# Optimization experiments

Measured on AMD Instinct MI355X. Metric: run time of the kernel, lower is better.

Reference implementation:

```python
import jax, jax.numpy as jnp
import numpy as np

E = 64          # num_experts
TOPK = 8        # num_experts_per_tok
I = 512         # moe_intermediate_size
H = 1024        # hidden_size
G = 128         # awq group_size
T = 2048        # tokens (batch*seq)

# AWQ nibble unpack order: bit shifts [0,16,4,20,8,24,12,28] -> indices [0,4,1,5,2,6,3,7]
_AWQ_SHIFTS = jnp.array([0, 4, 1, 5, 2, 6, 3, 7], dtype=jnp.int32) * 4


def awq_dequant(qw, qz, scales, group_size=G):
    """qw: (K, N//8) int32, qz: (K//G, N//8) int32, scales: (K//G, N) float.
    Returns dense weight (K, N): (q - z) * scale with per-group zero/scale."""
    K = qw.shape[0]
    uq = ((qw[:, :, None] >> _AWQ_SHIFTS) & 0xF).reshape(K, -1)          # (K, N)
    uz = ((qz[:, :, None] >> _AWQ_SHIFTS) & 0xF).reshape(qz.shape[0], -1)  # (K//G, N)
    uz = jnp.repeat(uz, group_size, axis=0)                               # (K, N)
    sc = jnp.repeat(scales, group_size, axis=0)                           # (K, N)
    return (uq.astype(scales.dtype) - uz.astype(scales.dtype)) * sc


def setup_inputs() -> dict:
    key = jax.random.key(0)
    ks = jax.random.split(key, 8)
    imax = 2**31 - 1
    return {
        "x": jax.random.normal(ks[0], (T, H), dtype=jnp.float32),
        "gate_w": jax.random.normal(ks[1], (E, H), dtype=jnp.float32) * 0.02,
        "qweight1": jax.random.randint(ks[2], (H, (E * I) // 8), 0, imax, dtype=jnp.int32),
        "qzeros1": jax.random.randint(ks[3], (H // G, (E * I) // 8), 0, imax, dtype=jnp.int32),
        "scales1": jax.random.normal(ks[4], (H // G, E * I), dtype=jnp.float32) * 0.02,
        "qweight2": jax.random.randint(ks[5], (I, (E * H) // 8), 0, imax, dtype=jnp.int32),
        "qzeros2": jax.random.randint(ks[6], (I // G, (E * H) // 8), 0, imax, dtype=jnp.int32),
        "scales2": jax.random.normal(ks[7], (I // G, E * H), dtype=jnp.float32) * 0.02,
    }


def reference(x, gate_w, qweight1, qzeros1, scales1, qweight2, qzeros2, scales2):
    # dequant grouped expert weights
    w1 = awq_dequant(qweight1, qzeros1, scales1).T.reshape(E, I, H)   # (E, I, H)
    w2 = awq_dequant(qweight2, qzeros2, scales2).T.reshape(E, H, I)   # (E, H, I)

    # routing: softmax -> top-k -> renormalize
    logits = x @ gate_w.T                                             # (T, E)
    probs = jax.nn.softmax(logits, axis=-1)
    topv, topi = jax.lax.top_k(probs, TOPK)                           # (T, K)
    topv = topv / jnp.sum(topv, axis=-1, keepdims=True)
    cw = jnp.sum(jax.nn.one_hot(topi, E, dtype=x.dtype) * topv[..., None], axis=1)  # (T, E)

    # experts: out = sum_e cw[t,e] * silu(x @ w1[e].T) @ w2[e].T
    h = jax.nn.silu(jnp.einsum('th,eih->tei', x, w1))                 # (T, E, I)
    h = h * cw[:, :, None]                                            # fold combine weights
    out = jnp.einsum('tei,ehi->th', h, w2)                            # (T, H)
    return out
```

## Files before the change

kernel.cpp:

```cpp
#include <hip/hip_runtime.h>
#include <hip/hip_bf16.h>

#define T_TOK 2048
#define HID   1024
#define EXP   64
#define TOPK  8
#define IMED  512
#define N1 (EXP * IMED)
#define C1 (N1 / 8)
#define N2 (EXP * HID)
#define C2 (N2 / 8)
#define MAXTILES 320

typedef _Float16 h16x2 __attribute__((ext_vector_type(2)));
typedef _Float16 h16x8 __attribute__((ext_vector_type(8)));
typedef float f32x4 __attribute__((ext_vector_type(4)));
typedef unsigned short ushortx4 __attribute__((ext_vector_type(4)));
typedef unsigned short ushortx8 __attribute__((ext_vector_type(8)));

__constant__ int kShifts[8] = {0, 16, 4, 20, 8, 24, 12, 28};

__device__ __forceinline__ void async16(const void* g, void* l) {
  __builtin_amdgcn_global_load_lds((const __attribute__((address_space(1))) void*)g,
                                   (__attribute__((address_space(3))) void*)l, 16, 0, 0);
}

__device__ __forceinline__ unsigned short f2h(float f) {
  return __builtin_bit_cast(unsigned short, (_Float16)f);
}
__device__ __forceinline__ float h2f(unsigned short b) {
  return (float)__builtin_bit_cast(_Float16, b);
}

__device__ __forceinline__ h16x8 unpack8h(unsigned q, h16x2 sh2, h16x2 zh2) {
  union { unsigned u[4]; h16x8 v; } out;
#pragma unroll
  for (int j = 0; j < 4; ++j) {
    const unsigned m = ((q >> (4 * j)) & 0x000F000Fu) | 0x64006400u;
    h16x2 d = __builtin_bit_cast(h16x2, m) - zh2;
    d = d * sh2;
    out.u[j] = __builtin_bit_cast(unsigned, d);
  }
  return out.v;
}

__device__ __forceinline__ void repack_body(const int* __restrict__ qw,
                                            unsigned* __restrict__ qk, int K, int C,
                                            int gx, int pp, int tid) {
  const int t = pp >> 2, fq = pp & 3;
  const int c2 = gx * 512 + tid * 2;
  const int nblk = c2 >> 1;
  unsigned o0[16], o1[16];
#pragma unroll
  for (int i = 0; i < 16; ++i) { o0[i] = 0u; o1[i] = 0u; }
  const int k0a = t * 64 + fq * 8;
  const int k0b = t * 64 + (fq + 4) * 8;
#pragma unroll
  for (int r = 0; r < 8; ++r) {
    const int2 va = *reinterpret_cast<const int2*>(qw + (size_t)(k0a + r) * C + c2);
    const int2 vb = *reinterpret_cast<const int2*>(qw + (size_t)(k0b + r) * C + c2);
    const int outsh = (r & 1) * 16 + (r >> 1) * 4;
    const unsigned qa[2] = {(unsigned)va.x, (unsigned)va.y};
    const unsigned qb[2] = {(unsigned)vb.x, (unsigned)vb.y};
#pragma unroll
    for (int ci = 0; ci < 2; ++ci) {
#pragma unroll
      for (int j = 0; j < 8; ++j) {
        const int sh = kShifts[j];
        o0[ci * 8 + j] |= ((qa[ci] >> sh) & 0xFu) << outsh;
        o1[ci * 8 + j] |= ((qb[ci] >> sh) & 0xFu) << outsh;
      }
    }
  }
  unsigned* dst = qk + (size_t)nblk * 2 * K + t * 128 + fq * 32;
#pragma unroll
  for (int idx = 0; idx < 16; ++idx)
    *reinterpret_cast<uint2*>(dst + idx * 2) = make_uint2(o0[idx], o1[idx]);
}

__global__ __launch_bounds__(256) void prep_kernel(
    const float* __restrict__ x, const float* __restrict__ gate_w,
    unsigned short* __restrict__ xh, float* __restrict__ partial,
    const int* __restrict__ qw1, unsigned* __restrict__ qk1,
    const int* __restrict__ qw2, unsigned* __restrict__ qk2,
    int* __restrict__ counts) {
  const int bid = blockIdx.x;
  const int tid = threadIdx.x;
  if (bid == 1535 && tid < 64) counts[tid] = 0;
  if (bid < 512) {
    __shared__ float xs[64][64];
    __shared__ float gs[64][64];
    const int t0 = (bid & 31) * 64;
    const int ks = bid >> 5;
    const int k0 = ks * 64;
    const int lrow = tid >> 4;
    const int cblk = tid & 15;
#pragma unroll
    for (int r = 0; r < 4; ++r) {
      const int row = r * 16 + lrow;
      const int sc = (cblk ^ ((row >> 2) & 15)) * 4;
      float4 xv = *reinterpret_cast<const float4*>(x + (size_t)(t0 + row) * HID + k0 + cblk * 4);
      float4 gv = *reinterpret_cast<const float4*>(gate_w + (size_t)row * HID + k0 + cblk * 4);
      *reinterpret_cast<float4*>(&xs[row][sc]) = xv;
      *reinterpret_cast<float4*>(&gs[row][sc]) = gv;
      ushortx4 o;
      o[0] = f2h(xv.x); o[1] = f2h(xv.y); o[2] = f2h(xv.z); o[3] = f2h(xv.w);
      *reinterpret_cast<ushortx4*>(xh + (size_t)(t0 + row) * HID + k0 + cblk * 4) = o;
    }
    __syncthreads();
    const int tg = (tid >> 4) * 4, eg = (tid & 15) * 4;
    const int xsw = tid >> 4, gsw = tid & 15;
    float acc[4][4] = {{0.f, 0.f, 0.f, 0.f}};
#pragma unroll 4
    for (int c = 0; c < 16; ++c) {
      float4 a[4], b[4];
#pragma unroll
      for (int i = 0; i < 4; ++i)
        a[i] = *reinterpret_cast<const float4*>(&xs[tg + i][(c ^ xsw) * 4]);
#pragma unroll
      for (int j = 0; j < 4; ++j)
        b[j] = *reinterpret_cast<const float4*>(&gs[eg + j][(c ^ gsw) * 4]);
#pragma unroll
      for (int i = 0; i < 4; ++i)
#pragma unroll
        for (int j = 0; j < 4; ++j) {
          acc[i][j] = fmaf(a[i].x, b[j].x, acc[i][j]);
          acc[i][j] = fmaf(a[i].y, b[j].y, acc[i][j]);
          acc[i][j] = fmaf(a[i].z, b[j].z, acc[i][j]);
          acc[i][j] = fmaf(a[i].w, b[j].w, acc[i][j]);
        }
    }
    float* dst = partial + ((size_t)ks * T_TOK + t0) * EXP;
#pragma unroll
    for (int i = 0; i < 4; ++i)
      *reinterpret_cast<float4*>(dst + (tg + i) * EXP + eg) =
          make_float4(acc[i][0], acc[i][1], acc[i][2], acc[i][3]);
  } else if (bid < 1024) {
    const int id = bid - 512;
    repack_body(qw1, qk1, HID, C1, id & 7, id >> 3, tid);
  } else {
    const int id = bid - 1024;
    repack_body(qw2, qk2, IMED, C2, id & 15, id >> 4, tid);
  }
}

__global__ __launch_bounds__(256) void topk_kernel(
    const float* __restrict__ partial, int* __restrict__ counts,
    int* __restrict__ tok_list, int* __restrict__ hslot_list,
    float* __restrict__ cw_list) {
  const int wave = threadIdx.x >> 6, lane = threadIdx.x & 63;
  const int t = blockIdx.x * 4 + wave;
  float lg = 0.f;
#pragma unroll
  for (int s = 0; s < 16; ++s)
    lg += partial[((size_t)s * T_TOK + t) * EXP + lane];

  float m = lg;
  for (int off = 32; off; off >>= 1) m = fmaxf(m, __shfl_xor(m, off));
  float pe = expf(lg - m);
  float s = pe;
  for (int off = 32; off; off >>= 1) s += __shfl_xor(s, off);
  float prob = pe / s;

  float pcur = prob;
  float myv = 0.f;
  int myi = -1;
  float tsum = 0.f;
  for (int k = 0; k < TOPK; ++k) {
    float vv = pcur;
    int idx = lane;
    for (int off = 32; off; off >>= 1) {
      float ov = __shfl_xor(vv, off);
      int oi = __shfl_xor(idx, off);
      if (ov > vv || (ov == vv && oi < idx)) { vv = ov; idx = oi; }
    }
    tsum += vv;
    if (lane == k) { myv = vv; myi = idx; }
    if (lane == idx) pcur = -1.f;
  }

  if (lane < TOPK) {
    const float cw = myv / tsum;
    const int ex = myi;
    const int slot = atomicAdd(&counts[ex], 1);
    tok_list[ex * T_TOK + slot] = t;
    hslot_list[ex * T_TOK + slot] = t * TOPK + lane;
    cw_list[ex * T_TOK + slot] = cw;
  }
}

#define TILE_LOOKUP(counts_ptr)                                            \
  __shared__ int sh_tl[4];                                                 \
  {                                                                        \
    if (threadIdx.x < 64) {                                                \
      const int n_ = (counts_ptr)[threadIdx.x];                            \
      const int nt_ = (n_ + 63) >> 6;                                      \
      int off_ = nt_;                                                      \
      for (int d_ = 1; d_ < 64; d_ <<= 1) {                                \
        const int v_ = __shfl_up(off_, d_);                                \
        if ((int)threadIdx.x >= d_) off_ += v_;                            \
      }                                                                    \
      const int excl_ = off_ - nt_;                                        \
      const int y_ = blockIdx.y;                                           \
      if (y_ >= excl_ && y_ < excl_ + nt_) {                               \
        sh_tl[0] = threadIdx.x; sh_tl[1] = (y_ - excl_) * 64; sh_tl[2] = n_; \
      }                                                                    \
      if (threadIdx.x == 63) sh_tl[3] = excl_ + nt_;                       \
    }                                                                      \
    __syncthreads();                                                       \
  }                                                                        \
  if ((int)blockIdx.y >= sh_tl[3]) return;                                 \
  const int e = sh_tl[0], t0 = sh_tl[1], n_e = sh_tl[2];

__global__ __launch_bounds__(256) void mfma_gemm1(
    const unsigned short* __restrict__ xh, const unsigned* __restrict__ qk1,
    const int* __restrict__ qz1, const float* __restrict__ sc1,
    const int* __restrict__ counts, const int* __restrict__ tok_list,
    const int* __restrict__ hslot_list, const float* __restrict__ cw_list,
    unsigned short* __restrict__ h_buf) {
  TILE_LOOKUP(counts)
  const int ntile = blockIdx.x;
  const int tid = threadIdx.x;
  const int wave = tid >> 6, lane = tid & 63;
  const int fr = lane & 15, fq = lane >> 4;

  __shared__ unsigned short As[2][64 * 64];

  const int arow = tid >> 3;
  const int acb = ((tid & 7) ^ ((tid >> 3) & 7)) * 16;
  const int ta0 = tok_list[e * T_TOK + min(t0 + arow, n_e - 1)];
  const int ta1 = tok_list[e * T_TOK + min(t0 + 32 + arow, n_e - 1)];
  const char* ga0 = (const char*)(xh + (size_t)ta0 * HID) + acb;
  const char* ga1 = (const char*)(xh + (size_t)ta1 * HID) + acb;

  auto stage = [&](int b) {
    char* l = (char*)&As[b][0] + wave * 1024;
    async16(ga0, l);
    async16(ga1, l + 4096);
    ga0 += 128; ga1 += 128;
  };

  const int nbase = e * IMED + ntile * 64 + wave * 16;
  const unsigned* bp = qk1 + (size_t)(nbase >> 4) * (2 * HID) + fq * 32 + fr * 2;
  const int col = nbase + fr;
  const int shz = ((fr >> 1) & 3) * 4 + (fr & 1) * 16;

  f32x4 acc[4];
#pragma unroll
  for (int i = 0; i < 4; ++i) acc[i] = (f32x4){0.f, 0.f, 0.f, 0.f};

  stage(0);
  uint2 qcur = *reinterpret_cast<const uint2*>(bp);
  float s_cur = sc1[col];
  unsigned zd_cur = (unsigned)qz1[col >> 3];
  int p = 0;
#pragma unroll 1
  for (int g = 0; g < HID / 128; ++g) {
    const unsigned shb = (unsigned)f2h(s_cur);
    const h16x2 sh2 = __builtin_bit_cast(h16x2, shb | (shb << 16));
    const unsigned zb = 0x6400u | ((zd_cur >> shz) & 15u);
    const h16x2 zh2 = __builtin_bit_cast(h16x2, zb | (zb << 16));
    float s_nxt = 0.f; unsigned zd_nxt = 0u;
#pragma unroll
    for (int hh = 0; hh < 2; ++hh) {
      const int t = g * 2 + hh;
      __syncthreads();
      if (t + 1 < HID / 64) stage(p ^ 1);
      uint2 qnext = make_uint2(0u, 0u);
      if (t + 1 < HID / 64) qnext = *reinterpret_cast<const uint2*>(bp + (t + 1) * 128);
      if (hh == 1 && g + 1 < HID / 128) {
        s_nxt = sc1[(size_t)(g + 1) * N1 + col];
        zd_nxt = (unsigned)qz1[(size_t)(g + 1) * C1 + (col >> 3)];
      }
      const h16x8 b0 = unpack8h(qcur.x, sh2, zh2);
      const h16x8 b1 = unpack8h(qcur.y, sh2, zh2);
#pragma unroll
      for (int kk = 0; kk < 2; ++kk) {
        const h16x8 bb = kk ? b1 : b0;
#pragma unroll
        for (int i = 0; i < 4; ++i) {
          const int row = i * 16 + fr;
          const h16x8 a = *reinterpret_cast<const h16x8*>(
              &As[p][row * 64 + (((kk * 4 + fq) ^ (fr & 7)) * 8)]);
          acc[i] = __builtin_amdgcn_mfma_f32_16x16x32_f16(a, bb, acc[i], 0, 0, 0);
        }
      }
      qcur = qnext; p ^= 1;
    }
    s_cur = s_nxt; zd_cur = zd_nxt;
  }

#pragma unroll
  for (int i = 0; i < 4; ++i) {
#pragma unroll
    for (int r = 0; r < 4; ++r) {
      const int grow = t0 + i * 16 + fq * 4 + r;
      if (grow < n_e) {
        const float cw = cw_list[e * T_TOK + grow];
        const int hs = hslot_list[e * T_TOK + grow];
        const float v = acc[i][r];
        h_buf[(size_t)hs * IMED + ntile * 64 + wave * 16 + fr] =
            f2h((v / (1.f + expf(-v))) * cw);
      }
    }
  }
}

__global__ __launch_bounds__(256) void mfma_gemm2(
    const unsigned short* __restrict__ h_buf, const unsigned* __restrict__ qk2,
    const int* __restrict__ qz2, const float* __restrict__ sc2,
    const int* __restrict__ counts, const int* __restrict__ hslot_list,
    unsigned short* __restrict__ p_buf) {
  TILE_LOOKUP(counts)
  const int ntile = blockIdx.x;
  const int tid = threadIdx.x;
  const int wave = tid >> 6, lane = tid & 63;
  const int fr = lane & 15, fq = lane >> 4;

  __shared__ unsigned short As[2][64 * 64];

  const int arow = tid >> 3;
  const int acb = ((tid & 7) ^ ((tid >> 3) & 7)) * 16;
  const int ha0 = hslot_list[e * T_TOK + min(t0 + arow, n_e - 1)];
  const int ha1 = hslot_list[e * T_TOK + min(t0 + 32 + arow, n_e - 1)];
  const char* ga0 = (const char*)(h_buf + (size_t)ha0 * IMED) + acb;
  const char* ga1 = (const char*)(h_buf + (size_t)ha1 * IMED) + acb;

  auto stage = [&](int b) {
    char* l = (char*)&As[b][0] + wave * 1024;
    async16(ga0, l);
    async16(ga1, l + 4096);
    ga0 += 128; ga1 += 128;
  };

  const int nbase = e * HID + ntile * 64 + wave * 16;
  const unsigned* bp = qk2 + (size_t)(nbase >> 4) * (2 * IMED) + fq * 32 + fr * 2;
  const int col = nbase + fr;
  const int shz = ((fr >> 1) & 3) * 4 + (fr & 1) * 16;

  f32x4 acc[4];
#pragma unroll
  for (int i = 0; i < 4; ++i) acc[i] = (f32x4){0.f, 0.f, 0.f, 0.f};

  stage(0);
  uint2 qcur = *reinterpret_cast<const uint2*>(bp);
  float s_cur = sc2[col];
  unsigned zd_cur = (unsigned)qz2[col >> 3];
  int p = 0;
#pragma unroll 1
  for (int g = 0; g < IMED / 128; ++g) {
    const unsigned shb = (unsigned)f2h(s_cur);
    const h16x2 sh2 = __builtin_bit_cast(h16x2, shb | (shb << 16));
    const unsigned zb = 0x6400u | ((zd_cur >> shz) & 15u);
    const h16x2 zh2 = __builtin_bit_cast(h16x2, zb | (zb << 16));
    float s_nxt = 0.f; unsigned zd_nxt = 0u;
#pragma unroll
    for (int hh = 0; hh < 2; ++hh) {
      const int t = g * 2 + hh;
      __syncthreads();
      if (t + 1 < IMED / 64) stage(p ^ 1);
      uint2 qnext = make_uint2(0u, 0u);
      if (t + 1 < IMED / 64) qnext = *reinterpret_cast<const uint2*>(bp + (t + 1) * 128);
      if (hh == 1 && g + 1 < IMED / 128) {
        s_nxt = sc2[(size_t)(g + 1) * N2 + col];
        zd_nxt = (unsigned)qz2[(size_t)(g + 1) * C2 + (col >> 3)];
      }
      const h16x8 b0 = unpack8h(qcur.x, sh2, zh2);
      const h16x8 b1 = unpack8h(qcur.y, sh2, zh2);
#pragma unroll
      for (int kk = 0; kk < 2; ++kk) {
        const h16x8 bb = kk ? b1 : b0;
#pragma unroll
        for (int i = 0; i < 4; ++i) {
          const int row = i * 16 + fr;
          const h16x8 a = *reinterpret_cast<const h16x8*>(
              &As[p][row * 64 + (((kk * 4 + fq) ^ (fr & 7)) * 8)]);
          acc[i] = __builtin_amdgcn_mfma_f32_16x16x32_f16(a, bb, acc[i], 0, 0, 0);
        }
      }
      qcur = qnext; p ^= 1;
    }
    s_cur = s_nxt; zd_cur = zd_nxt;
  }

#pragma unroll
  for (int i = 0; i < 4; ++i) {
#pragma unroll
    for (int r = 0; r < 4; ++r) {
      const int grow = t0 + i * 16 + fq * 4 + r;
      if (grow < n_e) {
        const int hs = hslot_list[e * T_TOK + grow];
        p_buf[(size_t)hs * HID + ntile * 64 + wave * 16 + fr] = f2h(acc[i][r]);
      }
    }
  }
}

__global__ __launch_bounds__(256) void reduce_kernel(const unsigned short* __restrict__ p_buf,
                                                     float* __restrict__ out) {
  const int idx = blockIdx.x * 256 + threadIdx.x;
  const int t = idx >> 7;
  const int c0 = (idx & 127) * 8;
  float s[8] = {0.f, 0.f, 0.f, 0.f, 0.f, 0.f, 0.f, 0.f};
#pragma unroll
  for (int k = 0; k < TOPK; ++k) {
    ushortx8 v = *reinterpret_cast<const ushortx8*>(p_buf + ((size_t)t * TOPK + k) * HID + c0);
#pragma unroll
    for (int j = 0; j < 8; ++j) s[j] += h2f(v[j]);
  }
  float* dst = out + (size_t)t * HID + c0;
  *reinterpret_cast<float4*>(dst) = make_float4(s[0], s[1], s[2], s[3]);
  *reinterpret_cast<float4*>(dst + 4) = make_float4(s[4], s[5], s[6], s[7]);
}

extern "C" void kernel_launch(void* const* d_in, const int* in_sizes, int n_in,
                              void* d_out, int out_size, void* d_ws, size_t ws_size,
                              hipStream_t stream) {
  const float* x      = (const float*)d_in[0];
  const float* gate_w = (const float*)d_in[1];
  const int*   qw1    = (const int*)d_in[2];
  const int*   qz1    = (const int*)d_in[3];
  const float* sc1    = (const float*)d_in[4];
  const int*   qw2    = (const int*)d_in[5];
  const int*   qz2    = (const int*)d_in[6];
  const float* sc2    = (const float*)d_in[7];
  float* out = (float*)d_out;

  char* ws = (char*)d_ws;
  int* counts           = (int*)(ws);
  int* tok_list         = (int*)(ws + 256);
  int* hslot_list       = (int*)(ws + 524544);
  float* cw_list        = (float*)(ws + 1048832);
  unsigned short* h_buf = (unsigned short*)(ws + 1573120);
  unsigned short* xh    = (unsigned short*)(ws + 18350336);
  unsigned* qk1         = (unsigned*)(ws + 22544640);
  unsigned* qk2         = (unsigned*)(ws + 39321856);
  unsigned short* p_buf = (unsigned short*)(ws + 56099072);
  float* partial        = (float*)(ws + 56099072);

  prep_kernel<<<1536, 256, 0, stream>>>(x, gate_w, xh, partial, qw1, qk1, qw2, qk2, counts);
  topk_kernel<<<T_TOK / 4, 256, 0, stream>>>(partial, counts, tok_list, hslot_list, cw_list);

  mfma_gemm1<<<dim3(IMED / 64, MAXTILES), 256, 0, stream>>>(
      xh, qk1, qz1, sc1, counts, tok_list, hslot_list, cw_list, h_buf);
  mfma_gemm2<<<dim3(HID / 64, MAXTILES), 256, 0, stream>>>(
      h_buf, qk2, qz2, sc2, counts, hslot_list, p_buf);
  reduce_kernel<<<(T_TOK * HID / 8) / 256, 256, 0, stream>>>(p_buf, out);
}
```

Baseline: 243.5 us.

## Load A fragments directly from global into registers, dropping LDS staging

Both MoE GEMM kernels stop staging the activation tile through double-buffered shared memory with async global-to-LDS copies and barriers. Each wave now loads its own A fragments straight from global memory into registers, with a one-step register prefetch. This removes the __syncthreads and LDS traffic. The cost is that the four waves, which share the same A rows, now each read them redundantly from global or L2, and register pressure rises.

Result: slower. 488.6 us (+100.6%).

```diff
diff --git a/kernel.cpp b/kernel.cpp
--- a/kernel.cpp
+++ b/kernel.cpp
@@ -19,11 +19,6 @@
 typedef unsigned short ushortx8 __attribute__((ext_vector_type(8)));
 
 __constant__ int kShifts[8] = {0, 16, 4, 20, 8, 24, 12, 28};
-
-__device__ __forceinline__ void async16(const void* g, void* l) {
-  __builtin_amdgcn_global_load_lds((const __attribute__((address_space(1))) void*)g,
-                                   (__attribute__((address_space(3))) void*)l, 16, 0, 0);
-}
 
 __device__ __forceinline__ unsigned short f2h(float f) {
   return __builtin_bit_cast(unsigned short, (_Float16)f);
@@ -224,21 +219,12 @@
   const int wave = tid >> 6, lane = tid & 63;
   const int fr = lane & 15, fq = lane >> 4;
 
-  __shared__ unsigned short As[2][64 * 64];
-
-  const int arow = tid >> 3;
-  const int acb = ((tid & 7) ^ ((tid >> 3) & 7)) * 16;
-  const int ta0 = tok_list[e * T_TOK + min(t0 + arow, n_e - 1)];
-  const int ta1 = tok_list[e * T_TOK + min(t0 + 32 + arow, n_e - 1)];
-  const char* ga0 = (const char*)(xh + (size_t)ta0 * HID) + acb;
-  const char* ga1 = (const char*)(xh + (size_t)ta1 * HID) + acb;
-
-  auto stage = [&](int b) {
-    char* l = (char*)&As[b][0] + wave * 1024;
-    async16(ga0, l);
-    async16(ga1, l + 4096);
-    ga0 += 128; ga1 += 128;
-  };
+  const unsigned short* ap[4];
+#pragma unroll
+  for (int i = 0; i < 4; ++i) {
+    const int ta = tok_list[e * T_TOK + min(t0 + i * 16 + fr, n_e - 1)];
+    ap[i] = xh + (size_t)ta * HID + fq * 8;
+  }
 
   const int nbase = e * IMED + ntile * 64 + wave * 16;
   const unsigned* bp = qk1 + (size_t)(nbase >> 4) * (2 * HID) + fq * 32 + fr * 2;
@@ -249,11 +235,15 @@
 #pragma unroll
   for (int i = 0; i < 4; ++i) acc[i] = (f32x4){0.f, 0.f, 0.f, 0.f};
 
-  stage(0);
+  h16x8 a0[4], a1[4];
+#pragma unroll
+  for (int i = 0; i < 4; ++i) {
+    a0[i] = *reinterpret_cast<const h16x8*>(ap[i]);
+    a1[i] = *reinterpret_cast<const h16x8*>(ap[i] + 32);
+  }
   uint2 qcur = *reinterpret_cast<const uint2*>(bp);
   float s_cur = sc1[col];
   unsigned zd_cur = (unsigned)qz1[col >> 3];
-  int p = 0;
 #pragma unroll 1
   for (int g = 0; g < HID / 128; ++g) {
     const unsigned shb = (unsigned)f2h(s_cur);
@@ -264,8 +254,13 @@
 #pragma unroll
     for (int hh = 0; hh < 2; ++hh) {
       const int t = g * 2 + hh;
-      __syncthreads();
-      if (t + 1 < HID / 64) stage(p ^ 1);
+      const int tn = (t + 1 < HID / 64) ? (t + 1) : t;
+      h16x8 n0[4], n1[4];
+#pragma unroll
+      for (int i = 0; i < 4; ++i) {
+        n0[i] = *reinterpret_cast<const h16x8*>(ap[i] + tn * 64);
+        n1[i] = *reinterpret_cast<const h16x8*>(ap[i] + tn * 64 + 32);
+      }
       uint2 qnext = make_uint2(0u, 0u);
       if (t + 1 < HID / 64) qnext = *reinterpret_cast<const uint2*>(bp + (t + 1) * 128);
       if (hh == 1 && g + 1 < HID / 128) {
@@ -275,17 +270,14 @@
       const h16x8 b0 = unpack8h(qcur.x, sh2, zh2);
       const h16x8 b1 = unpack8h(qcur.y, sh2, zh2);
 #pragma unroll
-      for (int kk = 0; kk < 2; ++kk) {
-        const h16x8 bb = kk ? b1 : b0;
-#pragma unroll
-        for (int i = 0; i < 4; ++i) {
-          const int row = i * 16 + fr;
-          const h16x8 a = *reinterpret_cast<const h16x8*>(
-              &As[p][row * 64 + (((kk * 4 + fq) ^ (fr & 7)) * 8)]);
-          acc[i] = __builtin_amdgcn_mfma_f32_16x16x32_f16(a, bb, acc[i], 0, 0, 0);
-        }
-      }
-      qcur = qnext; p ^= 1;
+      for (int i = 0; i < 4; ++i)
+        acc[i] = __builtin_amdgcn_mfma_f32_16x16x32_f16(a0[i], b0, acc[i], 0, 0, 0);
+#pragma unroll
+      for (int i = 0; i < 4; ++i)
+        acc[i] = __builtin_amdgcn_mfma_f32_16x16x32_f16(a1[i], b1, acc[i], 0, 0, 0);
+#pragma unroll
+      for (int i = 0; i < 4; ++i) { a0[i] = n0[i]; a1[i] = n1[i]; }
+      qcur = qnext;
     }
     s_cur = s_nxt; zd_cur = zd_nxt;
   }
@@ -317,21 +309,12 @@
   const int wave = tid >> 6, lane = tid & 63;
   const int fr = lane & 15, fq = lane >> 4;
 
-  __shared__ unsigned short As[2][64 * 64];
-
-  const int arow = tid >> 3;
-  const int acb = ((tid & 7) ^ ((tid >> 3) & 7)) * 16;
-  const int ha0 = hslot_list[e * T_TOK + min(t0 + arow, n_e - 1)];
-  const int ha1 = hslot_list[e * T_TOK + min(t0 + 32 + arow, n_e - 1)];
-  const char* ga0 = (const char*)(h_buf + (size_t)ha0 * IMED) + acb;
-  const char* ga1 = (const char*)(h_buf + (size_t)ha1 * IMED) + acb;
-
-  auto stage = [&](int b) {
-    char* l = (char*)&As[b][0] + wave * 1024;
-    async16(ga0, l);
-    async16(ga1, l + 4096);
-    ga0 += 128; ga1 += 128;
-  };
+  const unsigned short* ap[4];
+#pragma unroll
+  for (int i = 0; i < 4; ++i) {
+    const int ha = hslot_list[e * T_TOK + min(t0 + i * 16 + fr, n_e - 1)];
+    ap[i] = h_buf + (size_t)ha * IMED + fq * 8;
+  }
 
   const int nbase = e * HID + ntile * 64 + wave * 16;
   const unsigned* bp = qk2 + (size_t)(nbase >> 4) * (2 * IMED) + fq * 32 + fr * 2;
@@ -342,11 +325,15 @@
 #pragma unroll
   for (int i = 0; i < 4; ++i) acc[i] = (f32x4){0.f, 0.f, 0.f, 0.f};
 
-  stage(0);
+  h16x8 a0[4], a1[4];
+#pragma unroll
+  for (int i = 0; i < 4; ++i) {
+    a0[i] = *reinterpret_cast<const h16x8*>(ap[i]);
+    a1[i] = *reinterpret_cast<const h16x8*>(ap[i] + 32);
+  }
   uint2 qcur = *reinterpret_cast<const uint2*>(bp);
   float s_cur = sc2[col];
   unsigned zd_cur = (unsigned)qz2[col >> 3];
-  int p = 0;
 #pragma unroll 1
   for (int g = 0; g < IMED / 128; ++g) {
     const unsigned shb = (unsigned)f2h(s_cur);
@@ -357,8 +344,13 @@
 #pragma unroll
     for (int hh = 0; hh < 2; ++hh) {
       const int t = g * 2 + hh;
-      __syncthreads();
-      if (t + 1 < IMED / 64) stage(p ^ 1);
+      const int tn = (t + 1 < IMED / 64) ? (t + 1) : t;
+      h16x8 n0[4], n1[4];
+#pragma unroll
+      for (int i = 0; i < 4; ++i) {
+        n0[i] = *reinterpret_cast<const h16x8*>(ap[i] + tn * 64);
+        n1[i] = *reinterpret_cast<const h16x8*>(ap[i] + tn * 64 + 32);
+      }
       uint2 qnext = make_uint2(0u, 0u);
       if (t + 1 < IMED / 64) qnext = *reinterpret_cast<const uint2*>(bp + (t + 1) * 128);
       if (hh == 1 && g + 1 < IMED / 128) {
@@ -368,17 +360,14 @@
       const h16x8 b0 = unpack8h(qcur.x, sh2, zh2);
       const h16x8 b1 = unpack8h(qcur.y, sh2, zh2);
 #pragma unroll
-      for (int kk = 0; kk < 2; ++kk) {
-        const h16x8 bb = kk ? b1 : b0;
-#pragma unroll
-        for (int i = 0; i < 4; ++i) {
-          const int row = i * 16 + fr;
-          const h16x8 a = *reinterpret_cast<const h16x8*>(
-              &As[p][row * 64 + (((kk * 4 + fq) ^ (fr & 7)) * 8)]);
-          acc[i] = __builtin_amdgcn_mfma_f32_16x16x32_f16(a, bb, acc[i], 0, 0, 0);
-        }
-      }
-      qcur = qnext; p ^= 1;
+      for (int i = 0; i < 4; ++i)
+        acc[i] = __builtin_amdgcn_mfma_f32_16x16x32_f16(a0[i], b0, acc[i], 0, 0, 0);
+#pragma unroll
+      for (int i = 0; i < 4; ++i)
+        acc[i] = __builtin_amdgcn_mfma_f32_16x16x32_f16(a1[i], b1, acc[i], 0, 0, 0);
+#pragma unroll
+      for (int i = 0; i < 4; ++i) { a0[i] = n0[i]; a1[i] = n1[i]; }
+      qcur = qnext;
     }
     s_cur = s_nxt; zd_cur = zd_nxt;
   }
```
